# Performance work log

Hardware: AMD Instinct MI355X
Metric: run time of the kernel (lower is better)

The kernel has to match this reference:

```python
import jax, jax.numpy as jnp
import numpy as np

GRID = 256

def _build_edges(g):
    ii, jj = np.meshgrid(np.arange(g), np.arange(g), indexing='ij')
    center = ii * g + jj
    srcs, tgts, attrs = [], [], []
    for di in (-1, 0, 1):
        for dj in (-1, 0, 1):
            if di == 0 and dj == 0:
                continue
            ni, nj = ii + di, jj + dj
            m = (ni >= 0) & (ni < g) & (nj >= 0) & (nj < g)
            srcs.append(center[m])
            tgts.append((ni * g + nj)[m])
            n = int(m.sum())
            a = np.empty((n, 3), np.float32)
            a[:, 0] = np.sqrt(di * di + dj * dj)
            a[:, 1] = di
            a[:, 2] = dj
            attrs.append(a)
    return (np.concatenate(srcs).astype(np.int32),
            np.concatenate(tgts).astype(np.int32),
            np.concatenate(attrs, axis=0))

def setup_inputs() -> dict:
    key = jax.random.key(0)
    ks = jax.random.split(key, 16)
    B, T, C, g = 2, 5, 10, GRID
    width, kw, out_c, Hh = 64, 32, 10, 32
    src, tgt, attr = _build_edges(g)
    nrm = lambda k, s: 0.1 * jax.random.normal(k, s, dtype=jnp.float32)
    return {
        'x': nrm(ks[0], (B, T, C, g, g)),
        'edge_src': jnp.asarray(src),
        'edge_tgt': jnp.asarray(tgt),
        'edge_attr': jnp.asarray(attr),
        'Wih0': nrm(ks[1], (4 * Hh, C)),
        'Whh0': nrm(ks[2], (4 * Hh, Hh)),
        'bih0': nrm(ks[3], (4 * Hh,)),
        'bhh0': nrm(ks[4], (4 * Hh,)),
        'Wih1': nrm(ks[5], (4 * Hh, Hh)),
        'Whh1': nrm(ks[6], (4 * Hh, Hh)),
        'bih1': nrm(ks[7], (4 * Hh,)),
        'bhh1': nrm(ks[8], (4 * Hh,)),
        'fc1_w': nrm(ks[9], (width, Hh)),
        'fc1_b': nrm(ks[10], (width,)),
        'conv_w': nrm(ks[11], (4, width, width)),
        'conv_b': nrm(ks[12], (4, width)),
        'gparam': jnp.ones((4,), jnp.float32),
        'fc2_w': nrm(ks[13], (kw, width)),
        'fc2_b': nrm(ks[14], (kw,)),
        'fc3_w': nrm(ks[15], (out_c, kw)),
        'fc3_b': jnp.zeros((out_c,), jnp.float32),
    }

def _lstm_cell(xt, h, c, Wih, Whh, bih, bhh):
    z = xt @ Wih.T + bih + h @ Whh.T + bhh
    i, f, g, o = jnp.split(z, 4, axis=-1)  # torch gate order i,f,g,o
    c = jax.nn.sigmoid(f) * c + jax.nn.sigmoid(i) * jnp.tanh(g)
    h = jax.nn.sigmoid(o) * jnp.tanh(c)
    return h, c

def _forward(x, edge_src, edge_tgt, edge_attr, Wih0, Whh0, bih0, bhh0,
             Wih1, Whh1, bih1, bhh1, fc1_w, fc1_b, conv_w, conv_b, gparam,
             fc2_w, fc2_b, fc3_w, fc3_b):
    B, T, C, H, W = x.shape
    N = H * W
    Hh = Whh0.shape[1]
    # (B,T,C,H,W) -> (T, B*N, C) sequence for the temporal LSTM over every node
    seq = x.transpose(0, 3, 4, 1, 2).reshape(B * N, T, C).transpose(1, 0, 2)

    def step(carry, xt):
        h0, c0, h1, c1 = carry
        h0, c0 = _lstm_cell(xt, h0, c0, Wih0, Whh0, bih0, bhh0)
        h1, c1 = _lstm_cell(h0, h1, c1, Wih1, Whh1, bih1, bhh1)
        return (h0, c0, h1, c1), None

    z = jnp.zeros((B * N, Hh), x.dtype)
    (h0, c0, h1, c1), _ = jax.lax.scan(step, (z, z, z, z), seq)
    feats = jax.nn.relu(h1 @ fc1_w.T + fc1_b).reshape(B, N, -1)  # (B,N,width)

    dist2 = edge_attr[:, 0:1] ** 2  # (E,1)
    depth = conv_w.shape[0]
    for k in range(depth):
        gw = jnp.exp(-dist2 / (gparam[k] ** 2 + 1e-8))       # (E,1) gaussian gate
        msg = (feats[:, edge_src] @ conv_w[k]) * gw          # (B,E,width)
        agg = jnp.zeros_like(feats).at[:, edge_tgt].add(msg) # scatter-add per batch
        feats = agg + feats @ conv_w[k] + conv_b[k]
        if k != depth - 1:
            feats = jax.nn.relu(feats)

    out = jax.nn.relu(feats @ fc2_w.T + fc2_b) @ fc3_w.T + fc3_b  # (B,N,out_c)
    out = out.reshape(B, H, W, -1).transpose(0, 3, 1, 2)[:, None]  # (B,1,out_c,H,W)
    return out

def reference(x, edge_src, edge_tgt, edge_attr, Wih0, Whh0, bih0, bhh0,
              Wih1, Whh1, bih1, bhh1, fc1_w, fc1_b, conv_w, conv_b, gparam,
              fc2_w, fc2_b, fc3_w, fc3_b):
    return _forward(x, edge_src, edge_tgt, edge_attr, Wih0, Whh0, bih0, bhh0,
                    Wih1, Whh1, bih1, bhh1, fc1_w, fc1_b, conv_w, conv_b, gparam,
                    fc2_w, fc2_b, fc3_w, fc3_b)
```

## Files before the change

kernel.cpp:

```cpp
#include <hip/hip_runtime.h>
#include <hip/hip_bf16.h>

#define NPIX   65536
#define TT     5
#define CC     10
#define HH     32
#define WIDTH  64
#define KW     32
#define OUTC   10

#define OFF_L0I    0
#define OFF_L0H    1280
#define OFF_L1I    5376
#define OFF_L1H    9472
#define OFF_B0     13568
#define OFF_B1     13696
#define OFF_FC1W   13824
#define OFF_FC1B   15872
#define OFF_CWT2   16384
#define OFF_CB     32768
#define OFF_FC2W2  33024
#define OFF_FC2B   35072
#define OFF_FC3W4  35104
#define OFF_FC3B   35424
#define OFF_GW     35440
#define OFF_FEATS_A 36864
#define OFF_FEATS_B (36864 + 8388608)

#define STRAIGHT_ATTR_IDX (65025 * 3)

__device__ __forceinline__ float sigf(float x)  { return 1.0f / (1.0f + __expf(-x)); }
__device__ __forceinline__ float tanhf_(float x){ return 1.0f - 2.0f / (__expf(2.0f * x) + 1.0f); }

__global__ __launch_bounds__(256, 1)
void prep_kernel(const float* Wih0, const float* Whh0,
                 const float* bih0, const float* bhh0,
                 const float* Wih1, const float* Whh1,
                 const float* bih1, const float* bhh1,
                 const float* fc1w, const float* fc1b,
                 const float* convw, const float* convb,
                 const float* fc2w, const float* fc2b,
                 const float* fc3w, const float* fc3b,
                 const float* gparam, const float* eattr,
                 float* P) {
    int tid = blockIdx.x * blockDim.x + threadIdx.x;
    int stride = gridDim.x * blockDim.x;
    for (int idx = tid; idx < 1280; idx += stride) {
        int g = idx & 3, j = (idx >> 2) & 31, c = idx >> 7;
        P[OFF_L0I + idx] = Wih0[(g * 32 + j) * 10 + c];
    }
    for (int idx = tid; idx < 4096; idx += stride) {
        int g = idx & 3, j = (idx >> 2) & 31, k = idx >> 7;
        P[OFF_L0H + idx] = Whh0[(g * 32 + j) * 32 + k];
        P[OFF_L1I + idx] = Wih1[(g * 32 + j) * 32 + k];
        P[OFF_L1H + idx] = Whh1[(g * 32 + j) * 32 + k];
    }
    for (int idx = tid; idx < 128; idx += stride) {
        int g = idx & 3, j = idx >> 2;
        P[OFF_B0 + idx] = bih0[g * 32 + j] + bhh0[g * 32 + j];
        P[OFF_B1 + idx] = bih1[g * 32 + j] + bhh1[g * 32 + j];
    }
    for (int idx = tid; idx < 2048; idx += stride) {
        int ch = idx & 63, k = idx >> 6;
        P[OFF_FC1W + idx] = fc1w[ch * 32 + k];
    }
    for (int i = tid; i < 64; i += stride) P[OFF_FC1B + i] = fc1b[i];
    for (int idx = tid; idx < 16384; idx += stride) {
        int k = idx >> 12, r = idx & 4095, e = r >> 1, h = r & 1;
        int co2 = e >> 6, ci = e & 63;
        P[OFF_CWT2 + idx] = convw[k * 4096 + ci * 64 + (2 * co2 + h)];
    }
    for (int i = tid; i < 256; i += stride) P[OFF_CB + i] = convb[i];
    for (int idx = tid; idx < 2048; idx += stride) {
        int e = idx >> 1, h = idx & 1, m2 = e >> 6, ch = e & 63;
        P[OFF_FC2W2 + idx] = fc2w[(2 * m2 + h) * 64 + ch];
    }
    for (int i = tid; i < 32;  i += stride) P[OFF_FC2B + i] = fc2b[i];
    for (int idx = tid; idx < 320; idx += stride) {
        int q = idx & 3, e = idx >> 2, oc2 = e >> 4, m2 = e & 15;
        int oc = 2 * oc2 + (q & 1), m = 2 * m2 + (q >> 1);
        P[OFF_FC3W4 + idx] = fc3w[oc * 32 + m];
    }
    for (int i = tid; i < 10; i += stride) P[OFF_FC3B + i] = fc3b[i];
    for (int idx = tid; idx < 8; idx += stride) {
        int k = idx >> 1;
        float g = gparam[k];
        float denom = g * g + 1e-8f;
        float a = (idx & 1) ? eattr[0] : eattr[STRAIGHT_ATTR_IDX];
        P[OFF_GW + idx] = __expf(-(a * a) / denom);
    }
}

__global__ __launch_bounds__(128, 1)
void lstm_fc1_kernel(const float* __restrict__ x,
                     const float* __restrict__ P,
                     float* __restrict__ feats) {
    __shared__ float XS[CC * 128];
    __shared__ float H0[HH * 128];
    __shared__ float H1[HH * 128];

    int tid = threadIdx.x;
    int n = blockIdx.x * 128 + tid;
    int b = n >> 16;
    int pix = n & (NPIX - 1);
    const float* xb = x + (size_t)b * TT * CC * NPIX + pix;

    float4 z[HH];
    float c0[HH], c1[HH];
#pragma unroll
    for (int j = 0; j < HH; j++) {
        c0[j] = 0.f; c1[j] = 0.f;
        H0[j * 128 + tid] = 0.f;
        H1[j * 128 + tid] = 0.f;
    }

#pragma unroll 1
    for (int t = 0; t < TT; t++) {
#pragma unroll
        for (int c = 0; c < CC; c++)
            XS[c * 128 + tid] = xb[(size_t)(t * CC + c) * NPIX];

#pragma unroll
        for (int j = 0; j < HH; j++) z[j] = *(const float4*)(P + OFF_B0 + 4 * j);
#pragma unroll 1
        for (int c = 0; c < CC; c++) {
            float xv = XS[c * 128 + tid];
            const float* wr = P + OFF_L0I + c * 128;
#pragma unroll
            for (int j = 0; j < HH; j++) {
                z[j].x = __builtin_fmaf(wr[4 * j + 0], xv, z[j].x);
                z[j].y = __builtin_fmaf(wr[4 * j + 1], xv, z[j].y);
                z[j].z = __builtin_fmaf(wr[4 * j + 2], xv, z[j].z);
                z[j].w = __builtin_fmaf(wr[4 * j + 3], xv, z[j].w);
            }
        }
#pragma unroll 1
        for (int k = 0; k < HH; k++) {
            float hv = H0[k * 128 + tid];
            const float* wr = P + OFF_L0H + k * 128;
#pragma unroll
            for (int j = 0; j < HH; j++) {
                z[j].x = __builtin_fmaf(wr[4 * j + 0], hv, z[j].x);
                z[j].y = __builtin_fmaf(wr[4 * j + 1], hv, z[j].y);
                z[j].z = __builtin_fmaf(wr[4 * j + 2], hv, z[j].z);
                z[j].w = __builtin_fmaf(wr[4 * j + 3], hv, z[j].w);
            }
        }
#pragma unroll
        for (int j = 0; j < HH; j++) {
            float cn = sigf(z[j].y) * c0[j] + sigf(z[j].x) * tanhf_(z[j].z);
            c0[j] = cn;
            H0[j * 128 + tid] = sigf(z[j].w) * tanhf_(cn);
        }

#pragma unroll
        for (int j = 0; j < HH; j++) z[j] = *(const float4*)(P + OFF_B1 + 4 * j);
#pragma unroll 1
        for (int k = 0; k < HH; k++) {
            float hv = H0[k * 128 + tid];
            const float* wr = P + OFF_L1I + k * 128;
#pragma unroll
            for (int j = 0; j < HH; j++) {
                z[j].x = __builtin_fmaf(wr[4 * j + 0], hv, z[j].x);
                z[j].y = __builtin_fmaf(wr[4 * j + 1], hv, z[j].y);
                z[j].z = __builtin_fmaf(wr[4 * j + 2], hv, z[j].z);
                z[j].w = __builtin_fmaf(wr[4 * j + 3], hv, z[j].w);
            }
        }
#pragma unroll 1
        for (int k = 0; k < HH; k++) {
            float hv = H1[k * 128 + tid];
            const float* wr = P + OFF_L1H + k * 128;
#pragma unroll
            for (int j = 0; j < HH; j++) {
                z[j].x = __builtin_fmaf(wr[4 * j + 0], hv, z[j].x);
                z[j].y = __builtin_fmaf(wr[4 * j + 1], hv, z[j].y);
                z[j].z = __builtin_fmaf(wr[4 * j + 2], hv, z[j].z);
                z[j].w = __builtin_fmaf(wr[4 * j + 3], hv, z[j].w);
            }
        }
#pragma unroll
        for (int j = 0; j < HH; j++) {
            float cn = sigf(z[j].y) * c1[j] + sigf(z[j].x) * tanhf_(z[j].z);
            c1[j] = cn;
            H1[j * 128 + tid] = sigf(z[j].w) * tanhf_(cn);
        }
    }

    float f[WIDTH];
#pragma unroll
    for (int ch = 0; ch < WIDTH; ch++) f[ch] = P[OFF_FC1B + ch];
#pragma unroll 1
    for (int k = 0; k < HH; k++) {
        float hv = H1[k * 128 + tid];
        const float* wr = P + OFF_FC1W + k * 64;
#pragma unroll
        for (int ch = 0; ch < WIDTH; ch++)
            f[ch] = __builtin_fmaf(wr[ch], hv, f[ch]);
    }
    float* fb = feats + (size_t)b * WIDTH * NPIX + pix;
#pragma unroll
    for (int ch = 0; ch < WIDTH; ch++)
        fb[(size_t)ch * NPIX] = fmaxf(f[ch], 0.f);
}

__global__ __launch_bounds__(256, 1)
void conv_fused_kernel(const float* __restrict__ Fin, float* __restrict__ Fout,
                       const float* __restrict__ P, int k) {
    __shared__ float4 CW[1024];
    __shared__ float  CB[64];
    {
        const float4* src = (const float4*)(P + OFF_CWT2 + k * 4096);
        for (int i = threadIdx.x; i < 1024; i += 256) CW[i] = src[i];
        if (threadIdx.x < 64) CB[threadIdx.x] = P[OFF_CB + k * 64 + threadIdx.x];
    }
    __syncthreads();

    int n = blockIdx.x * 256 + threadIdx.x;
    int b = n >> 16;
    int pix = n & (NPIX - 1);
    int i = pix >> 8, j = pix & 255;
    float wstr = P[OFF_GW + 2 * k], wdiag = P[OFF_GW + 2 * k + 1];
    float fu = (i > 0) ? wstr : 0.f, fd = (i < 255) ? wstr : 0.f;
    float fl = (j > 0) ? wstr : 0.f, fr = (j < 255) ? wstr : 0.f;
    float ful = (i > 0 && j > 0) ? wdiag : 0.f, fur = (i > 0 && j < 255) ? wdiag : 0.f;
    float fdl = (i < 255 && j > 0) ? wdiag : 0.f, fdr = (i < 255 && j < 255) ? wdiag : 0.f;

    const float* fb = Fin + (size_t)b * WIDTH * NPIX + pix;
    float u[WIDTH];
#pragma unroll
    for (int ch = 0; ch < WIDTH; ch++) {
        const float* yc = fb + (size_t)ch * NPIX;
        float v = yc[0];
        v += fu * yc[-256] + fd * yc[256] + fl * yc[-1] + fr * yc[1];
        v += ful * yc[-257] + fur * yc[-255] + fdl * yc[255] + fdr * yc[257];
        u[ch] = v;
    }

    float* ob = Fout + (size_t)b * WIDTH * NPIX + pix;
#pragma unroll 1
    for (int co2 = 0; co2 < 32; co2++) {
        float ax = CB[2 * co2], ay = CB[2 * co2 + 1];
        const float4* wv = CW + co2 * 32;
#pragma unroll
        for (int ci2 = 0; ci2 < 32; ci2++) {
            float4 q = wv[ci2];
            float a0 = u[2 * ci2], a1 = u[2 * ci2 + 1];
            ax = __builtin_fmaf(q.x, a0, ax); ax = __builtin_fmaf(q.z, a1, ax);
            ay = __builtin_fmaf(q.y, a0, ay); ay = __builtin_fmaf(q.w, a1, ay);
        }
        ob[(size_t)(2 * co2) * NPIX]     = fmaxf(ax, 0.f);
        ob[(size_t)(2 * co2 + 1) * NPIX] = fmaxf(ay, 0.f);
    }
}

__global__ __launch_bounds__(256, 1)
void conv_head_kernel(const float* __restrict__ Fin, const float* __restrict__ P,
                      float* __restrict__ out) {
    const int k = 3;
    __shared__ float4 CW3[1024];
    __shared__ float  CB3[64];
    __shared__ float4 F2W[512];
    __shared__ float  F2B[32];
    __shared__ float4 F3W[80];
    __shared__ float  F3B[12];
    {
        const float4* s1 = (const float4*)(P + OFF_CWT2 + k * 4096);
        for (int i = threadIdx.x; i < 1024; i += 256) CW3[i] = s1[i];
        const float4* s2 = (const float4*)(P + OFF_FC2W2);
        for (int i = threadIdx.x; i < 512; i += 256) F2W[i] = s2[i];
        const float4* s3 = (const float4*)(P + OFF_FC3W4);
        if (threadIdx.x < 80) F3W[threadIdx.x] = s3[threadIdx.x];
        if (threadIdx.x < 64) CB3[threadIdx.x] = P[OFF_CB + k * 64 + threadIdx.x];
        if (threadIdx.x < 32) F2B[threadIdx.x] = P[OFF_FC2B + threadIdx.x];
        if (threadIdx.x < 10) F3B[threadIdx.x] = P[OFF_FC3B + threadIdx.x];
    }
    __syncthreads();

    int n = blockIdx.x * 256 + threadIdx.x;
    int b = n >> 16;
    int pix = n & (NPIX - 1);
    int i = pix >> 8, j = pix & 255;
    float wstr = P[OFF_GW + 2 * k], wdiag = P[OFF_GW + 2 * k + 1];
    float fu = (i > 0) ? wstr : 0.f, fd = (i < 255) ? wstr : 0.f;
    float fl = (j > 0) ? wstr : 0.f, fr = (j < 255) ? wstr : 0.f;
    float ful = (i > 0 && j > 0) ? wdiag : 0.f, fur = (i > 0 && j < 255) ? wdiag : 0.f;
    float fdl = (i < 255 && j > 0) ? wdiag : 0.f, fdr = (i < 255 && j < 255) ? wdiag : 0.f;

    const float* fb = Fin + (size_t)b * WIDTH * NPIX + pix;
    float u[WIDTH];
#pragma unroll
    for (int ch = 0; ch < WIDTH; ch++) {
        const float* yc = fb + (size_t)ch * NPIX;
        float v = yc[0];
        v += fu * yc[-256] + fd * yc[256] + fl * yc[-1] + fr * yc[1];
        v += ful * yc[-257] + fur * yc[-255] + fdl * yc[255] + fdr * yc[257];
        u[ch] = v;
    }

    float f[WIDTH];
#pragma unroll
    for (int co2 = 0; co2 < 32; co2++) {
        float ax = CB3[2 * co2], ay = CB3[2 * co2 + 1];
        const float4* wv = CW3 + co2 * 32;
#pragma unroll
        for (int ci2 = 0; ci2 < 32; ci2++) {
            float4 q = wv[ci2];
            float a0 = u[2 * ci2], a1 = u[2 * ci2 + 1];
            ax = __builtin_fmaf(q.x, a0, ax); ax = __builtin_fmaf(q.z, a1, ax);
            ay = __builtin_fmaf(q.y, a0, ay); ay = __builtin_fmaf(q.w, a1, ay);
        }
        f[2 * co2] = ax; f[2 * co2 + 1] = ay;
    }

    float2 oo[5];
#pragma unroll
    for (int oc2 = 0; oc2 < 5; oc2++) oo[oc2] = make_float2(F3B[2 * oc2], F3B[2 * oc2 + 1]);
#pragma unroll 1
    for (int m2 = 0; m2 < 16; m2++) {
        float ax = F2B[2 * m2], ay = F2B[2 * m2 + 1];
        const float4* wv = F2W + m2 * 32;
#pragma unroll
        for (int ch2 = 0; ch2 < 32; ch2++) {
            float4 q = wv[ch2];
            ax = __builtin_fmaf(q.x, f[2 * ch2], ax); ax = __builtin_fmaf(q.z, f[2 * ch2 + 1], ax);
            ay = __builtin_fmaf(q.y, f[2 * ch2], ay); ay = __builtin_fmaf(q.w, f[2 * ch2 + 1], ay);
        }
        ax = fmaxf(ax, 0.f); ay = fmaxf(ay, 0.f);
#pragma unroll
        for (int oc2 = 0; oc2 < 5; oc2++) {
            float4 q = F3W[oc2 * 16 + m2];
            oo[oc2].x += q.x * ax + q.z * ay;
            oo[oc2].y += q.y * ax + q.w * ay;
        }
    }
    float* ob = out + (size_t)b * OUTC * NPIX + pix;
#pragma unroll
    for (int oc2 = 0; oc2 < 5; oc2++) {
        ob[(size_t)(2 * oc2) * NPIX]     = oo[oc2].x;
        ob[(size_t)(2 * oc2 + 1) * NPIX] = oo[oc2].y;
    }
}

extern "C" void kernel_launch(void* const* d_in, const int* in_sizes, int n_in,
                              void* d_out, int out_size, void* d_ws, size_t ws_size,
                              hipStream_t stream) {
    const float* x     = (const float*)d_in[0];
    const float* eattr = (const float*)d_in[3];
    const float* Wih0  = (const float*)d_in[4];
    const float* Whh0  = (const float*)d_in[5];
    const float* bih0  = (const float*)d_in[6];
    const float* bhh0  = (const float*)d_in[7];
    const float* Wih1  = (const float*)d_in[8];
    const float* Whh1  = (const float*)d_in[9];
    const float* bih1  = (const float*)d_in[10];
    const float* bhh1  = (const float*)d_in[11];
    const float* fc1w  = (const float*)d_in[12];
    const float* fc1b  = (const float*)d_in[13];
    const float* convw = (const float*)d_in[14];
    const float* convb = (const float*)d_in[15];
    const float* gparam= (const float*)d_in[16];
    const float* fc2w  = (const float*)d_in[17];
    const float* fc2b  = (const float*)d_in[18];
    const float* fc3w  = (const float*)d_in[19];
    const float* fc3b  = (const float*)d_in[20];

    float* P  = (float*)d_ws;
    float* FA = P + OFF_FEATS_A;
    float* FB = P + OFF_FEATS_B;

    prep_kernel<<<64, 256, 0, stream>>>(Wih0, Whh0, bih0, bhh0, Wih1, Whh1, bih1, bhh1,
                                        fc1w, fc1b, convw, convb, fc2w, fc2b, fc3w, fc3b,
                                        gparam, eattr, P);
    lstm_fc1_kernel<<<1024, 128, 0, stream>>>(x, P, FA);
    conv_fused_kernel<<<512, 256, 0, stream>>>(FA, FB, P, 0);
    conv_fused_kernel<<<512, 256, 0, stream>>>(FB, FA, P, 1);
    conv_fused_kernel<<<512, 256, 0, stream>>>(FA, FB, P, 2);
    conv_head_kernel<<<512, 256, 0, stream>>>(FB, P, (float*)d_out);
}
```

Measured before the change: 638.4 us.

## Split LSTM gates into groups, read conv weights from global, unfuse head

The LSTM step now computes gate pre-activations in four groups of 8 hidden units instead of all 32 at once. This shrinks the live accumulator set from 128 floats to 32 and buffers the new hidden state before writing it back, and the weight layout is repacked to match. The conv kernels drop the shared-memory weight staging and read uniform weights directly from global, expecting scalar loads. The last conv layer is split from the fc2/fc3 head into a separate kernel. The split adds one more full feature-map round trip through memory, and it may change how well the compiler schedules the weight reads.

```diff
diff --git a/kernel.cpp b/kernel.cpp
--- a/kernel.cpp
+++ b/kernel.cpp
@@ -17,11 +17,11 @@
 #define OFF_B1     13696
 #define OFF_FC1W   13824
 #define OFF_FC1B   15872
-#define OFF_CWT2   16384
+#define OFF_CWT    16384
 #define OFF_CB     32768
-#define OFF_FC2W2  33024
+#define OFF_FC2W   33024
 #define OFF_FC2B   35072
-#define OFF_FC3W4  35104
+#define OFF_FC3T   35104
 #define OFF_FC3B   35424
 #define OFF_GW     35440
 #define OFF_FEATS_A 36864
@@ -46,14 +46,17 @@
     int tid = blockIdx.x * blockDim.x + threadIdx.x;
     int stride = gridDim.x * blockDim.x;
     for (int idx = tid; idx < 1280; idx += stride) {
-        int g = idx & 3, j = (idx >> 2) & 31, c = idx >> 7;
-        P[OFF_L0I + idx] = Wih0[(g * 32 + j) * 10 + c];
+        int g = idx & 3, j8 = (idx >> 2) & 7, rest = idx >> 5;
+        int c = rest % 10, grp = rest / 10;
+        P[OFF_L0I + idx] = Wih0[(g * 32 + grp * 8 + j8) * 10 + c];
     }
     for (int idx = tid; idx < 4096; idx += stride) {
-        int g = idx & 3, j = (idx >> 2) & 31, k = idx >> 7;
-        P[OFF_L0H + idx] = Whh0[(g * 32 + j) * 32 + k];
-        P[OFF_L1I + idx] = Wih1[(g * 32 + j) * 32 + k];
-        P[OFF_L1H + idx] = Whh1[(g * 32 + j) * 32 + k];
+        int g = idx & 3, j8 = (idx >> 2) & 7, rest = idx >> 5;
+        int k = rest & 31, grp = rest >> 5;
+        int row = (g * 32 + grp * 8 + j8) * 32 + k;
+        P[OFF_L0H + idx] = Whh0[row];
+        P[OFF_L1I + idx] = Wih1[row];
+        P[OFF_L1H + idx] = Whh1[row];
     }
     for (int idx = tid; idx < 128; idx += stride) {
         int g = idx & 3, j = idx >> 2;
@@ -66,20 +69,15 @@
     }
     for (int i = tid; i < 64; i += stride) P[OFF_FC1B + i] = fc1b[i];
     for (int idx = tid; idx < 16384; idx += stride) {
-        int k = idx >> 12, r = idx & 4095, e = r >> 1, h = r & 1;
-        int co2 = e >> 6, ci = e & 63;
-        P[OFF_CWT2 + idx] = convw[k * 4096 + ci * 64 + (2 * co2 + h)];
+        int k = idx >> 12, r = idx & 4095, co = r >> 6, ci = r & 63;
+        P[OFF_CWT + idx] = convw[k * 4096 + ci * 64 + co];
     }
     for (int i = tid; i < 256; i += stride) P[OFF_CB + i] = convb[i];
-    for (int idx = tid; idx < 2048; idx += stride) {
-        int e = idx >> 1, h = idx & 1, m2 = e >> 6, ch = e & 63;
-        P[OFF_FC2W2 + idx] = fc2w[(2 * m2 + h) * 64 + ch];
-    }
+    for (int i = tid; i < 2048; i += stride) P[OFF_FC2W + i] = fc2w[i];
     for (int i = tid; i < 32;  i += stride) P[OFF_FC2B + i] = fc2b[i];
     for (int idx = tid; idx < 320; idx += stride) {
-        int q = idx & 3, e = idx >> 2, oc2 = e >> 4, m2 = e & 15;
-        int oc = 2 * oc2 + (q & 1), m = 2 * m2 + (q >> 1);
-        P[OFF_FC3W4 + idx] = fc3w[oc * 32 + m];
+        int m = idx / 10, oc = idx % 10;
+        P[OFF_FC3T + idx] = fc3w[oc * 32 + m];
     }
     for (int i = tid; i < 10; i += stride) P[OFF_FC3B + i] = fc3b[i];
     for (int idx = tid; idx < 8; idx += stride) {
@@ -105,13 +103,12 @@
     int pix = n & (NPIX - 1);
     const float* xb = x + (size_t)b * TT * CC * NPIX + pix;
 
-    float4 z[HH];
-    float c0[HH], c1[HH];
-#pragma unroll
-    for (int j = 0; j < HH; j++) {
-        c0[j] = 0.f; c1[j] = 0.f;
-        H0[j * 128 + tid] = 0.f;
-        H1[j * 128 + tid] = 0.f;
+    float c0[HH], c1[HH], hn[HH];
+#pragma unroll
+    for (int jj = 0; jj < HH; jj++) {
+        c0[jj] = 0.f; c1[jj] = 0.f;
+        H0[jj * 128 + tid] = 0.f;
+        H1[jj * 128 + tid] = 0.f;
     }
 
 #pragma unroll 1
@@ -121,70 +118,86 @@
             XS[c * 128 + tid] = xb[(size_t)(t * CC + c) * NPIX];
 
 #pragma unroll
-        for (int j = 0; j < HH; j++) z[j] = *(const float4*)(P + OFF_B0 + 4 * j);
-#pragma unroll 1
-        for (int c = 0; c < CC; c++) {
-            float xv = XS[c * 128 + tid];
-            const float* wr = P + OFF_L0I + c * 128;
-#pragma unroll
-            for (int j = 0; j < HH; j++) {
-                z[j].x = __builtin_fmaf(wr[4 * j + 0], xv, z[j].x);
-                z[j].y = __builtin_fmaf(wr[4 * j + 1], xv, z[j].y);
-                z[j].z = __builtin_fmaf(wr[4 * j + 2], xv, z[j].z);
-                z[j].w = __builtin_fmaf(wr[4 * j + 3], xv, z[j].w);
+        for (int grp = 0; grp < 4; grp++) {
+            float4 z[8];
+#pragma unroll
+            for (int j8 = 0; j8 < 8; j8++)
+                z[j8] = *(const float4*)(P + OFF_B0 + (grp * 8 + j8) * 4);
+#pragma unroll 1
+            for (int c = 0; c < CC; c++) {
+                float xv = XS[c * 128 + tid];
+                const float* wr = P + OFF_L0I + (grp * 10 + c) * 32;
+#pragma unroll
+                for (int j8 = 0; j8 < 8; j8++) {
+                    z[j8].x = __builtin_fmaf(wr[j8 * 4 + 0], xv, z[j8].x);
+                    z[j8].y = __builtin_fmaf(wr[j8 * 4 + 1], xv, z[j8].y);
+                    z[j8].z = __builtin_fmaf(wr[j8 * 4 + 2], xv, z[j8].z);
+                    z[j8].w = __builtin_fmaf(wr[j8 * 4 + 3], xv, z[j8].w);
+                }
+            }
+#pragma unroll 1
+            for (int k = 0; k < HH; k++) {
+                float hv = H0[k * 128 + tid];
+                const float* wr = P + OFF_L0H + (grp * 32 + k) * 32;
+#pragma unroll
+                for (int j8 = 0; j8 < 8; j8++) {
+                    z[j8].x = __builtin_fmaf(wr[j8 * 4 + 0], hv, z[j8].x);
+                    z[j8].y = __builtin_fmaf(wr[j8 * 4 + 1], hv, z[j8].y);
+                    z[j8].z = __builtin_fmaf(wr[j8 * 4 + 2], hv, z[j8].z);
+                    z[j8].w = __builtin_fmaf(wr[j8 * 4 + 3], hv, z[j8].w);
+                }
+            }
+#pragma unroll
+            for (int j8 = 0; j8 < 8; j8++) {
+                int j = grp * 8 + j8;
+                float cn = sigf(z[j8].y) * c0[j] + sigf(z[j8].x) * tanhf_(z[j8].z);
+                c0[j] = cn;
+                hn[j] = sigf(z[j8].w) * tanhf_(cn);
             }
         }
-#pragma unroll 1
-        for (int k = 0; k < HH; k++) {
-            float hv = H0[k * 128 + tid];
-            const float* wr = P + OFF_L0H + k * 128;
-#pragma unroll
-            for (int j = 0; j < HH; j++) {
-                z[j].x = __builtin_fmaf(wr[4 * j + 0], hv, z[j].x);
-                z[j].y = __builtin_fmaf(wr[4 * j + 1], hv, z[j].y);
-                z[j].z = __builtin_fmaf(wr[4 * j + 2], hv, z[j].z);
-                z[j].w = __builtin_fmaf(wr[4 * j + 3], hv, z[j].w);
+#pragma unroll
+        for (int jj = 0; jj < HH; jj++) H0[jj * 128 + tid] = hn[jj];
+
+#pragma unroll
+        for (int grp = 0; grp < 4; grp++) {
+            float4 z[8];
+#pragma unroll
+            for (int j8 = 0; j8 < 8; j8++)
+                z[j8] = *(const float4*)(P + OFF_B1 + (grp * 8 + j8) * 4);
+#pragma unroll 1
+            for (int k = 0; k < HH; k++) {
+                float hv = H0[k * 128 + tid];
+                const float* wr = P + OFF_L1I + (grp * 32 + k) * 32;
+#pragma unroll
+                for (int j8 = 0; j8 < 8; j8++) {
+                    z[j8].x = __builtin_fmaf(wr[j8 * 4 + 0], hv, z[j8].x);
+                    z[j8].y = __builtin_fmaf(wr[j8 * 4 + 1], hv, z[j8].y);
+                    z[j8].z = __builtin_fmaf(wr[j8 * 4 + 2], hv, z[j8].z);
+                    z[j8].w = __builtin_fmaf(wr[j8 * 4 + 3], hv, z[j8].w);
+                }
+            }
+#pragma unroll 1
+            for (int k = 0; k < HH; k++) {
+                float hv = H1[k * 128 + tid];
+                const float* wr = P + OFF_L1H + (grp * 32 + k) * 32;
+#pragma unroll
+                for (int j8 = 0; j8 < 8; j8++) {
+                    z[j8].x = __builtin_fmaf(wr[j8 * 4 + 0], hv, z[j8].x);
+                    z[j8].y = __builtin_fmaf(wr[j8 * 4 + 1], hv, z[j8].y);
+                    z[j8].z = __builtin_fmaf(wr[j8 * 4 + 2], hv, z[j8].z);
+                    z[j8].w = __builtin_fmaf(wr[j8 * 4 + 3], hv, z[j8].w);
+                }
+            }
+#pragma unroll
+            for (int j8 = 0; j8 < 8; j8++) {
+                int j = grp * 8 + j8;
+                float cn = sigf(z[j8].y) * c1[j] + sigf(z[j8].x) * tanhf_(z[j8].z);
+                c1[j] = cn;
+                hn[j] = sigf(z[j8].w) * tanhf_(cn);
             }
         }
 #pragma unroll
-        for (int j = 0; j < HH; j++) {
-            float cn = sigf(z[j].y) * c0[j] + sigf(z[j].x) * tanhf_(z[j].z);
-            c0[j] = cn;
-            H0[j * 128 + tid] = sigf(z[j].w) * tanhf_(cn);
-        }
-
-#pragma unroll
-        for (int j = 0; j < HH; j++) z[j] = *(const float4*)(P + OFF_B1 + 4 * j);
-#pragma unroll 1
-        for (int k = 0; k < HH; k++) {
-            float hv = H0[k * 128 + tid];
-            const float* wr = P + OFF_L1I + k * 128;
-#pragma unroll
-            for (int j = 0; j < HH; j++) {
-                z[j].x = __builtin_fmaf(wr[4 * j + 0], hv, z[j].x);
-                z[j].y = __builtin_fmaf(wr[4 * j + 1], hv, z[j].y);
-                z[j].z = __builtin_fmaf(wr[4 * j + 2], hv, z[j].z);
-                z[j].w = __builtin_fmaf(wr[4 * j + 3], hv, z[j].w);
-            }
-        }
-#pragma unroll 1
-        for (int k = 0; k < HH; k++) {
-            float hv = H1[k * 128 + tid];
-            const float* wr = P + OFF_L1H + k * 128;
-#pragma unroll
-            for (int j = 0; j < HH; j++) {
-                z[j].x = __builtin_fmaf(wr[4 * j + 0], hv, z[j].x);
-                z[j].y = __builtin_fmaf(wr[4 * j + 1], hv, z[j].y);
-                z[j].z = __builtin_fmaf(wr[4 * j + 2], hv, z[j].z);
-                z[j].w = __builtin_fmaf(wr[4 * j + 3], hv, z[j].w);
-            }
-        }
-#pragma unroll
-        for (int j = 0; j < HH; j++) {
-            float cn = sigf(z[j].y) * c1[j] + sigf(z[j].x) * tanhf_(z[j].z);
-            c1[j] = cn;
-            H1[j * 128 + tid] = sigf(z[j].w) * tanhf_(cn);
-        }
+        for (int jj = 0; jj < HH; jj++) H1[jj * 128 + tid] = hn[jj];
     }
 
     float f[WIDTH];
@@ -205,17 +218,8 @@
 }
 
 __global__ __launch_bounds__(256, 1)
-void conv_fused_kernel(const float* __restrict__ Fin, float* __restrict__ Fout,
-                       const float* __restrict__ P, int k) {
-    __shared__ float4 CW[1024];
-    __shared__ float  CB[64];
-    {
-        const float4* src = (const float4*)(P + OFF_CWT2 + k * 4096);
-        for (int i = threadIdx.x; i < 1024; i += 256) CW[i] = src[i];
-        if (threadIdx.x < 64) CB[threadIdx.x] = P[OFF_CB + k * 64 + threadIdx.x];
-    }
-    __syncthreads();
-
+void conv_mm_kernel(const float* __restrict__ Fin, float* __restrict__ Fout,
+                    const float* __restrict__ P, int k, int dorelu) {
     int n = blockIdx.x * 256 + threadIdx.x;
     int b = n >> 16;
     int pix = n & (NPIX - 1);
@@ -237,109 +241,50 @@
         u[ch] = v;
     }
 
+    const float* wbase = P + OFF_CWT + (k << 12);
+    const float* cb = P + OFF_CB + k * 64;
     float* ob = Fout + (size_t)b * WIDTH * NPIX + pix;
 #pragma unroll 1
-    for (int co2 = 0; co2 < 32; co2++) {
-        float ax = CB[2 * co2], ay = CB[2 * co2 + 1];
-        const float4* wv = CW + co2 * 32;
-#pragma unroll
-        for (int ci2 = 0; ci2 < 32; ci2++) {
-            float4 q = wv[ci2];
-            float a0 = u[2 * ci2], a1 = u[2 * ci2 + 1];
-            ax = __builtin_fmaf(q.x, a0, ax); ax = __builtin_fmaf(q.z, a1, ax);
-            ay = __builtin_fmaf(q.y, a0, ay); ay = __builtin_fmaf(q.w, a1, ay);
-        }
-        ob[(size_t)(2 * co2) * NPIX]     = fmaxf(ax, 0.f);
-        ob[(size_t)(2 * co2 + 1) * NPIX] = fmaxf(ay, 0.f);
+    for (int co = 0; co < 64; co++) {
+        const float* wr = wbase + co * 64;
+        float acc = cb[co];
+#pragma unroll
+        for (int ci = 0; ci < WIDTH; ci++)
+            acc = __builtin_fmaf(wr[ci], u[ci], acc);
+        ob[(size_t)co * NPIX] = dorelu ? fmaxf(acc, 0.f) : acc;
     }
 }
 
 __global__ __launch_bounds__(256, 1)
-void conv_head_kernel(const float* __restrict__ Fin, const float* __restrict__ P,
-                      float* __restrict__ out) {
-    const int k = 3;
-    __shared__ float4 CW3[1024];
-    __shared__ float  CB3[64];
-    __shared__ float4 F2W[512];
-    __shared__ float  F2B[32];
-    __shared__ float4 F3W[80];
-    __shared__ float  F3B[12];
-    {
-        const float4* s1 = (const float4*)(P + OFF_CWT2 + k * 4096);
-        for (int i = threadIdx.x; i < 1024; i += 256) CW3[i] = s1[i];
-        const float4* s2 = (const float4*)(P + OFF_FC2W2);
-        for (int i = threadIdx.x; i < 512; i += 256) F2W[i] = s2[i];
-        const float4* s3 = (const float4*)(P + OFF_FC3W4);
-        if (threadIdx.x < 80) F3W[threadIdx.x] = s3[threadIdx.x];
-        if (threadIdx.x < 64) CB3[threadIdx.x] = P[OFF_CB + k * 64 + threadIdx.x];
-        if (threadIdx.x < 32) F2B[threadIdx.x] = P[OFF_FC2B + threadIdx.x];
-        if (threadIdx.x < 10) F3B[threadIdx.x] = P[OFF_FC3B + threadIdx.x];
-    }
-    __syncthreads();
-
+void head_kernel(const float* __restrict__ Fin, const float* __restrict__ P,
+                 float* __restrict__ out) {
     int n = blockIdx.x * 256 + threadIdx.x;
     int b = n >> 16;
     int pix = n & (NPIX - 1);
-    int i = pix >> 8, j = pix & 255;
-    float wstr = P[OFF_GW + 2 * k], wdiag = P[OFF_GW + 2 * k + 1];
-    float fu = (i > 0) ? wstr : 0.f, fd = (i < 255) ? wstr : 0.f;
-    float fl = (j > 0) ? wstr : 0.f, fr = (j < 255) ? wstr : 0.f;
-    float ful = (i > 0 && j > 0) ? wdiag : 0.f, fur = (i > 0 && j < 255) ? wdiag : 0.f;
-    float fdl = (i < 255 && j > 0) ? wdiag : 0.f, fdr = (i < 255 && j < 255) ? wdiag : 0.f;
-
     const float* fb = Fin + (size_t)b * WIDTH * NPIX + pix;
-    float u[WIDTH];
-#pragma unroll
-    for (int ch = 0; ch < WIDTH; ch++) {
-        const float* yc = fb + (size_t)ch * NPIX;
-        float v = yc[0];
-        v += fu * yc[-256] + fd * yc[256] + fl * yc[-1] + fr * yc[1];
-        v += ful * yc[-257] + fur * yc[-255] + fdl * yc[255] + fdr * yc[257];
-        u[ch] = v;
-    }
-
     float f[WIDTH];
 #pragma unroll
-    for (int co2 = 0; co2 < 32; co2++) {
-        float ax = CB3[2 * co2], ay = CB3[2 * co2 + 1];
-        const float4* wv = CW3 + co2 * 32;
-#pragma unroll
-        for (int ci2 = 0; ci2 < 32; ci2++) {
-            float4 q = wv[ci2];
-            float a0 = u[2 * ci2], a1 = u[2 * ci2 + 1];
-            ax = __builtin_fmaf(q.x, a0, ax); ax = __builtin_fmaf(q.z, a1, ax);
-            ay = __builtin_fmaf(q.y, a0, ay); ay = __builtin_fmaf(q.w, a1, ay);
-        }
-        f[2 * co2] = ax; f[2 * co2 + 1] = ay;
-    }
-
-    float2 oo[5];
-#pragma unroll
-    for (int oc2 = 0; oc2 < 5; oc2++) oo[oc2] = make_float2(F3B[2 * oc2], F3B[2 * oc2 + 1]);
-#pragma unroll 1
-    for (int m2 = 0; m2 < 16; m2++) {
-        float ax = F2B[2 * m2], ay = F2B[2 * m2 + 1];
-        const float4* wv = F2W + m2 * 32;
-#pragma unroll
-        for (int ch2 = 0; ch2 < 32; ch2++) {
-            float4 q = wv[ch2];
-            ax = __builtin_fmaf(q.x, f[2 * ch2], ax); ax = __builtin_fmaf(q.z, f[2 * ch2 + 1], ax);
-            ay = __builtin_fmaf(q.y, f[2 * ch2], ay); ay = __builtin_fmaf(q.w, f[2 * ch2 + 1], ay);
-        }
-        ax = fmaxf(ax, 0.f); ay = fmaxf(ay, 0.f);
-#pragma unroll
-        for (int oc2 = 0; oc2 < 5; oc2++) {
-            float4 q = F3W[oc2 * 16 + m2];
-            oo[oc2].x += q.x * ax + q.z * ay;
-            oo[oc2].y += q.y * ax + q.w * ay;
-        }
+    for (int ch = 0; ch < WIDTH; ch++) f[ch] = fb[(size_t)ch * NPIX];
+
+    float oo[OUTC];
+#pragma unroll
+    for (int oc = 0; oc < OUTC; oc++) oo[oc] = P[OFF_FC3B + oc];
+#pragma unroll 1
+    for (int m = 0; m < KW; m++) {
+        const float* wr = P + OFF_FC2W + m * 64;
+        float a = P[OFF_FC2B + m];
+#pragma unroll
+        for (int ch = 0; ch < WIDTH; ch++)
+            a = __builtin_fmaf(wr[ch], f[ch], a);
+        a = fmaxf(a, 0.f);
+        const float* w3 = P + OFF_FC3T + m * 10;
+#pragma unroll
+        for (int oc = 0; oc < OUTC; oc++)
+            oo[oc] = __builtin_fmaf(w3[oc], a, oo[oc]);
     }
     float* ob = out + (size_t)b * OUTC * NPIX + pix;
 #pragma unroll
-    for (int oc2 = 0; oc2 < 5; oc2++) {
-        ob[(size_t)(2 * oc2) * NPIX]     = oo[oc2].x;
-        ob[(size_t)(2 * oc2 + 1) * NPIX] = oo[oc2].y;
-    }
+    for (int oc = 0; oc < OUTC; oc++) ob[(size_t)oc * NPIX] = oo[oc];
 }
 
 extern "C" void kernel_launch(void* const* d_in, const int* in_sizes, int n_in,
@@ -373,8 +318,9 @@
                                         fc1w, fc1b, convw, convb, fc2w, fc2b, fc3w, fc3b,
                                         gparam, eattr, P);
     lstm_fc1_kernel<<<1024, 128, 0, stream>>>(x, P, FA);
-    conv_fused_kernel<<<512, 256, 0, stream>>>(FA, FB, P, 0);
-    conv_fused_kernel<<<512, 256, 0, stream>>>(FB, FA, P, 1);
-    conv_fused_kernel<<<512, 256, 0, stream>>>(FA, FB, P, 2);
-    conv_head_kernel<<<512, 256, 0, stream>>>(FB, P, (float*)d_out);
-}
+    conv_mm_kernel<<<512, 256, 0, stream>>>(FA, FB, P, 0, 1);
+    conv_mm_kernel<<<512, 256, 0, stream>>>(FB, FA, P, 1, 1);
+    conv_mm_kernel<<<512, 256, 0, stream>>>(FA, FB, P, 2, 1);
+    conv_mm_kernel<<<512, 256, 0, stream>>>(FB, FA, P, 3, 0);
+    head_kernel<<<512, 256, 0, stream>>>(FA, P, (float*)d_out);
+}
```

Result: slower. 849.6 us (+33.1%).
